# Performance work log

Hardware: AMD Instinct MI355X
Metric: run time of the kernel (lower is better)

The kernel has to match this reference:

```python
import jax, jax.numpy as jnp
import numpy as np

B, T = 16384, 2048
NUM_TOKENS = 60   # |A5| = 60
ID_ID = 0         # identity element id
LOGIT_VAL = 5.0


def setup_inputs() -> dict:
    key = jax.random.key(0)
    k1, k2 = jax.random.split(key)
    input_ids = jax.random.randint(k1, (B, T), 0, NUM_TOKENS, dtype=jnp.int32)
    # Cayley table: mul[a, b] = a*b in the group. Any table with entries in
    # [0, 60) exercises identical compute; a real A5 table would be passed here.
    mul = jax.random.randint(k2, (NUM_TOKENS, NUM_TOKENS), 0, NUM_TOKENS, dtype=jnp.int32)
    return {"input_ids": input_ids, "mul": mul}


def reference(input_ids, mul):
    # Sequential left-fold over timesteps: s_{t+1} = mul[x_t, s_t]
    Bv = input_ids.shape[0]

    def step(s, xt):
        return mul[xt, s], None  # per-row gather mul[xt[i], s[i]]

    s0 = jnp.full((Bv,), ID_ID, dtype=input_ids.dtype)
    s, _ = jax.lax.scan(step, s0, input_ids.T)  # scan over T; carries [B]

    # one-hot logits scaled to 5.0 (torch scatter_ of constant 5.0)
    logits = jnp.zeros((Bv, NUM_TOKENS), dtype=jnp.float32)
    logits = logits.at[jnp.arange(Bv), s].set(LOGIT_VAL)
    return logits
```

## Files before the change

kernel.cpp:

```cpp
#include <hip/hip_runtime.h>


#define T_LEN 2048
#define NTOK 60
#define NPAIR (NTOK * NTOK)
#define ROW_WORDS 675
#define NWORDS (NTOK * ROW_WORDS)
#define ALLOC_WORDS (NWORDS + 4)
#define TAB_BYTES (ALLOC_WORDS * 4)
#define BROWS 64

__global__ void a5_build_kernel(const int* __restrict__ mul,
                                uint32_t* __restrict__ packed) {
  const int w = blockIdx.x * 256 + threadIdx.x;
  if (w >= ALLOC_WORDS) return;
  if (w >= NWORDS) { packed[w] = 0; return; }
  const uint32_t r = (uint32_t)w / ROW_WORDS;
  const uint32_t woff = (uint32_t)w - r * ROW_WORDS;
  const uint32_t bit0 = woff * 32u;
  const uint32_t e0 = bit0 / 6u;
  const uint32_t sh0 = bit0 - e0 * 6u;
  uint64_t acc = 0;
#pragma unroll
  for (int k = 0; k < 7; ++k) {
    const uint32_t e = e0 + k;
    if (e < NPAIR) {
      const uint32_t x1 = e % 60u;
      const uint32_t x2 = e / 60u;
      const uint32_t v =
          (uint32_t)mul[x2 * 60u + (uint32_t)mul[x1 * 60u + r]];
      acc |= (uint64_t)v << (6 * k);
    }
  }
  packed[w] = (uint32_t)(acc >> sh0);
}

__global__ __launch_bounds__(BROWS)
__attribute__((amdgpu_waves_per_eu(1, 1)))
void a5_scan2_kernel(const int* __restrict__ ids,
                     const uint32_t* __restrict__ packed,
                     float* __restrict__ out) {
  extern __shared__ uint32_t tab[];
  const int lane = threadIdx.x;

  {
    const uint4* s4 = (const uint4*)packed;
    uint4* d4 = (uint4*)tab;
#pragma unroll 4
    for (int i = lane; i < ALLOC_WORDS / 4; i += BROWS) d4[i] = s4[i];
  }
  __syncthreads();

  const int row = blockIdx.x * BROWS + lane;
  const int4* rp = (const int4*)(ids + (size_t)row * T_LEN);
  const char* tb = (const char*)tab;

  uint32_t s = 0;
  uint32_t po[8], shv[8];

#define PREP(J, X1, X2)                                           \
  do {                                                            \
    const uint32_t p6_ = (uint32_t)(X2)*360u + (uint32_t)(X1)*6u; \
    po[J] = (p6_ >> 5) << 2;                                      \
    shv[J] = p6_ & 31u;                                           \
  } while (0)

#define PSTEP(J)                                                  \
  do {                                                            \
    const uint32_t a_ = s * 2700u + po[J];                        \
    const uint32_t lo_ = *(const uint32_t*)(tb + a_);             \
    const uint32_t hi_ = *(const uint32_t*)(tb + a_ + 4);         \
    s = __builtin_amdgcn_alignbit(hi_, lo_, shv[J]) & 63u;        \
  } while (0)

  int4 n0, n1, n2, n3;
  {
    int4 c0 = rp[0], c1 = rp[1], c2 = rp[2], c3 = rp[3];
    PREP(0, c0.x, c0.y); PREP(1, c0.z, c0.w);
    PREP(2, c1.x, c1.y); PREP(3, c1.z, c1.w);
    PREP(4, c2.x, c2.y); PREP(5, c2.z, c2.w);
    PREP(6, c3.x, c3.y); PREP(7, c3.z, c3.w);
    n0 = rp[4]; n1 = rp[5]; n2 = rp[6]; n3 = rp[7];
  }

  for (int b = 0; b <= 125; ++b) {
    const int4* mp = rp + (size_t)(b + 2) * 4;
    int4 m0 = mp[0], m1 = mp[1], m2 = mp[2], m3 = mp[3];
    __builtin_amdgcn_sched_barrier(0);
    PSTEP(0); PSTEP(1); PSTEP(2); PSTEP(3);
    PSTEP(4); PSTEP(5); PSTEP(6); PSTEP(7);
    __builtin_amdgcn_sched_barrier(0);
    PREP(0, n0.x, n0.y); PREP(1, n0.z, n0.w);
    PREP(2, n1.x, n1.y); PREP(3, n1.z, n1.w);
    PREP(4, n2.x, n2.y); PREP(5, n2.z, n2.w);
    PREP(6, n3.x, n3.y); PREP(7, n3.z, n3.w);
    n0 = m0; n1 = m1; n2 = m2; n3 = m3;
  }
  PSTEP(0); PSTEP(1); PSTEP(2); PSTEP(3);
  PSTEP(4); PSTEP(5); PSTEP(6); PSTEP(7);
  PREP(0, n0.x, n0.y); PREP(1, n0.z, n0.w);
  PREP(2, n1.x, n1.y); PREP(3, n1.z, n1.w);
  PREP(4, n2.x, n2.y); PREP(5, n2.z, n2.w);
  PREP(6, n3.x, n3.y); PREP(7, n3.z, n3.w);
  PSTEP(0); PSTEP(1); PSTEP(2); PSTEP(3);
  PSTEP(4); PSTEP(5); PSTEP(6); PSTEP(7);
#undef PSTEP
#undef PREP

  float4* op = (float4*)(out + (size_t)row * NTOK);
#pragma unroll
  for (int j = 0; j < 15; ++j) {
    float4 v;
    v.x = ((uint32_t)(4 * j + 0) == s) ? 5.0f : 0.0f;
    v.y = ((uint32_t)(4 * j + 1) == s) ? 5.0f : 0.0f;
    v.z = ((uint32_t)(4 * j + 2) == s) ? 5.0f : 0.0f;
    v.w = ((uint32_t)(4 * j + 3) == s) ? 5.0f : 0.0f;
    op[j] = v;
  }
}

__global__ __launch_bounds__(BROWS, 1) void a5_scan_kernel(
    const int* __restrict__ ids, const int* __restrict__ mul,
    float* __restrict__ out) {
  __shared__ uint32_t tab[NTOK * NTOK];
  const int lane = threadIdx.x;
  for (int i = lane; i < NTOK * NTOK; i += BROWS)
    tab[i] = ((uint32_t)mul[i]) << 2;
  __syncthreads();

  const int row = blockIdx.x * BROWS + lane;
  const int4* rp = (const int4*)(ids + (size_t)row * T_LEN);
  const char* tb = (const char*)tab;
  int4 c0 = rp[0], c1 = rp[1], c2 = rp[2], c3 = rp[3];
  uint32_t s4 = 0;
#define STEP(X)                                  \
  do {                                           \
    uint32_t base_ = (uint32_t)(X)*240u;         \
    s4 = *(const uint32_t*)(tb + base_ + s4);    \
  } while (0)
  for (int t = 0; t < T_LEN; t += 16) {
    int4 q0, q1, q2, q3;
    const bool more = (t + 16) < T_LEN;
    if (more) {
      const int4* np = rp + (t >> 2) + 4;
      q0 = np[0]; q1 = np[1]; q2 = np[2]; q3 = np[3];
    }
    STEP(c0.x); STEP(c0.y); STEP(c0.z); STEP(c0.w);
    STEP(c1.x); STEP(c1.y); STEP(c1.z); STEP(c1.w);
    STEP(c2.x); STEP(c2.y); STEP(c2.z); STEP(c2.w);
    STEP(c3.x); STEP(c3.y); STEP(c3.z); STEP(c3.w);
    if (more) { c0 = q0; c1 = q1; c2 = q2; c3 = q3; }
  }
#undef STEP
  const uint32_t s = s4 >> 2;
  float4* op = (float4*)(out + (size_t)row * NTOK);
#pragma unroll
  for (int j = 0; j < 15; ++j) {
    float4 v;
    v.x = ((uint32_t)(4 * j + 0) == s) ? 5.0f : 0.0f;
    v.y = ((uint32_t)(4 * j + 1) == s) ? 5.0f : 0.0f;
    v.z = ((uint32_t)(4 * j + 2) == s) ? 5.0f : 0.0f;
    v.w = ((uint32_t)(4 * j + 3) == s) ? 5.0f : 0.0f;
    op[j] = v;
  }
}

extern "C" void kernel_launch(void* const* d_in, const int* in_sizes, int n_in,
                              void* d_out, int out_size, void* d_ws,
                              size_t ws_size, hipStream_t stream) {
  const int* ids = (const int*)d_in[0];
  const int* mul = (const int*)d_in[1];
  float* out = (float*)d_out;
  const int B = in_sizes[0] / T_LEN;
  const int grid = B / BROWS;

  if (ws_size >= (size_t)TAB_BYTES) {
    uint32_t* packed = (uint32_t*)d_ws;
    (void)hipFuncSetAttribute((const void*)a5_scan2_kernel,
                              hipFuncAttributeMaxDynamicSharedMemorySize,
                              TAB_BYTES);
    a5_build_kernel<<<(ALLOC_WORDS + 255) / 256, 256, 0, stream>>>(mul, packed);
    a5_scan2_kernel<<<grid, BROWS, TAB_BYTES, stream>>>(ids, packed, out);
  } else {
    a5_scan_kernel<<<grid, BROWS, 0, stream>>>(ids, mul, out);
  }
}
```

Measured before the change: 84.81 us.

## Process two independent rows per thread to interleave dependent LDS lookup chains

Each thread now scans two rows (tid and tid+8192) and alternates their dependent shared-memory lookup steps, so two independent chains hide each other's LDS latency. The grid is halved, which also halves the number of times the ~162KB packed table is copied into LDS. The cost is roughly double the register pressure and only 128 blocks on a GPU with many more CUs, which may leave compute units idle. The fast path now also requires B to equal exactly 16384.

```diff
diff --git a/kernel.cpp b/kernel.cpp
--- a/kernel.cpp
+++ b/kernel.cpp
@@ -9,6 +9,7 @@
 #define ALLOC_WORDS (NWORDS + 4)
 #define TAB_BYTES (ALLOC_WORDS * 4)
 #define BROWS 64
+#define HALF_B 8192
 
 __global__ void a5_build_kernel(const int* __restrict__ mul,
                                 uint32_t* __restrict__ packed) {
@@ -37,9 +38,9 @@
 
 __global__ __launch_bounds__(BROWS)
 __attribute__((amdgpu_waves_per_eu(1, 1)))
-void a5_scan2_kernel(const int* __restrict__ ids,
-                     const uint32_t* __restrict__ packed,
-                     float* __restrict__ out) {
+void a5_scan2x2_kernel(const int* __restrict__ ids,
+                       const uint32_t* __restrict__ packed,
+                       float* __restrict__ out) {
   extern __shared__ uint32_t tab[];
   const int lane = threadIdx.x;
 
@@ -51,71 +52,114 @@
   }
   __syncthreads();
 
-  const int row = blockIdx.x * BROWS + lane;
-  const int4* rp = (const int4*)(ids + (size_t)row * T_LEN);
+  const int tid = blockIdx.x * BROWS + lane;
+  const int4* rpA = (const int4*)(ids + (size_t)tid * T_LEN);
+  const int4* rpB = (const int4*)(ids + (size_t)(tid + HALF_B) * T_LEN);
   const char* tb = (const char*)tab;
 
-  uint32_t s = 0;
-  uint32_t po[8], shv[8];
-
-#define PREP(J, X1, X2)                                           \
+  uint32_t sA = 0, sB = 0;
+  uint32_t poA[8], shA[8], poB[8], shB[8];
+
+#define PREPC(PO, SH, J, X1, X2)                                  \
   do {                                                            \
     const uint32_t p6_ = (uint32_t)(X2)*360u + (uint32_t)(X1)*6u; \
-    po[J] = (p6_ >> 5) << 2;                                      \
-    shv[J] = p6_ & 31u;                                           \
+    PO[J] = (p6_ >> 5) << 2;                                      \
+    SH[J] = p6_ & 31u;                                            \
   } while (0)
 
-#define PSTEP(J)                                                  \
+#define PSTEPC(S, PO, SH, J)                                      \
   do {                                                            \
-    const uint32_t a_ = s * 2700u + po[J];                        \
+    const uint32_t a_ = S * 2700u + PO[J];                        \
     const uint32_t lo_ = *(const uint32_t*)(tb + a_);             \
     const uint32_t hi_ = *(const uint32_t*)(tb + a_ + 4);         \
-    s = __builtin_amdgcn_alignbit(hi_, lo_, shv[J]) & 63u;        \
+    S = __builtin_amdgcn_alignbit(hi_, lo_, SH[J]) & 63u;         \
   } while (0)
 
-  int4 n0, n1, n2, n3;
+  int4 nA0, nA1, nA2, nA3, nB0, nB1, nB2, nB3;
   {
-    int4 c0 = rp[0], c1 = rp[1], c2 = rp[2], c3 = rp[3];
-    PREP(0, c0.x, c0.y); PREP(1, c0.z, c0.w);
-    PREP(2, c1.x, c1.y); PREP(3, c1.z, c1.w);
-    PREP(4, c2.x, c2.y); PREP(5, c2.z, c2.w);
-    PREP(6, c3.x, c3.y); PREP(7, c3.z, c3.w);
-    n0 = rp[4]; n1 = rp[5]; n2 = rp[6]; n3 = rp[7];
+    int4 c0 = rpA[0], c1 = rpA[1], c2 = rpA[2], c3 = rpA[3];
+    PREPC(poA, shA, 0, c0.x, c0.y); PREPC(poA, shA, 1, c0.z, c0.w);
+    PREPC(poA, shA, 2, c1.x, c1.y); PREPC(poA, shA, 3, c1.z, c1.w);
+    PREPC(poA, shA, 4, c2.x, c2.y); PREPC(poA, shA, 5, c2.z, c2.w);
+    PREPC(poA, shA, 6, c3.x, c3.y); PREPC(poA, shA, 7, c3.z, c3.w);
+    int4 d0 = rpB[0], d1 = rpB[1], d2 = rpB[2], d3 = rpB[3];
+    PREPC(poB, shB, 0, d0.x, d0.y); PREPC(poB, shB, 1, d0.z, d0.w);
+    PREPC(poB, shB, 2, d1.x, d1.y); PREPC(poB, shB, 3, d1.z, d1.w);
+    PREPC(poB, shB, 4, d2.x, d2.y); PREPC(poB, shB, 5, d2.z, d2.w);
+    PREPC(poB, shB, 6, d3.x, d3.y); PREPC(poB, shB, 7, d3.z, d3.w);
+    nA0 = rpA[4]; nA1 = rpA[5]; nA2 = rpA[6]; nA3 = rpA[7];
+    nB0 = rpB[4]; nB1 = rpB[5]; nB2 = rpB[6]; nB3 = rpB[7];
   }
 
   for (int b = 0; b <= 125; ++b) {
-    const int4* mp = rp + (size_t)(b + 2) * 4;
-    int4 m0 = mp[0], m1 = mp[1], m2 = mp[2], m3 = mp[3];
+    const int4* mpA = rpA + (size_t)(b + 2) * 4;
+    const int4* mpB = rpB + (size_t)(b + 2) * 4;
+    int4 mA0 = mpA[0], mA1 = mpA[1], mA2 = mpA[2], mA3 = mpA[3];
+    int4 mB0 = mpB[0], mB1 = mpB[1], mB2 = mpB[2], mB3 = mpB[3];
     __builtin_amdgcn_sched_barrier(0);
-    PSTEP(0); PSTEP(1); PSTEP(2); PSTEP(3);
-    PSTEP(4); PSTEP(5); PSTEP(6); PSTEP(7);
+    PSTEPC(sA, poA, shA, 0); PSTEPC(sB, poB, shB, 0);
+    PSTEPC(sA, poA, shA, 1); PSTEPC(sB, poB, shB, 1);
+    PSTEPC(sA, poA, shA, 2); PSTEPC(sB, poB, shB, 2);
+    PSTEPC(sA, poA, shA, 3); PSTEPC(sB, poB, shB, 3);
+    PSTEPC(sA, poA, shA, 4); PSTEPC(sB, poB, shB, 4);
+    PSTEPC(sA, poA, shA, 5); PSTEPC(sB, poB, shB, 5);
+    PSTEPC(sA, poA, shA, 6); PSTEPC(sB, poB, shB, 6);
+    PSTEPC(sA, poA, shA, 7); PSTEPC(sB, poB, shB, 7);
     __builtin_amdgcn_sched_barrier(0);
-    PREP(0, n0.x, n0.y); PREP(1, n0.z, n0.w);
-    PREP(2, n1.x, n1.y); PREP(3, n1.z, n1.w);
-    PREP(4, n2.x, n2.y); PREP(5, n2.z, n2.w);
-    PREP(6, n3.x, n3.y); PREP(7, n3.z, n3.w);
-    n0 = m0; n1 = m1; n2 = m2; n3 = m3;
-  }
-  PSTEP(0); PSTEP(1); PSTEP(2); PSTEP(3);
-  PSTEP(4); PSTEP(5); PSTEP(6); PSTEP(7);
-  PREP(0, n0.x, n0.y); PREP(1, n0.z, n0.w);
-  PREP(2, n1.x, n1.y); PREP(3, n1.z, n1.w);
-  PREP(4, n2.x, n2.y); PREP(5, n2.z, n2.w);
-  PREP(6, n3.x, n3.y); PREP(7, n3.z, n3.w);
-  PSTEP(0); PSTEP(1); PSTEP(2); PSTEP(3);
-  PSTEP(4); PSTEP(5); PSTEP(6); PSTEP(7);
-#undef PSTEP
-#undef PREP
-
-  float4* op = (float4*)(out + (size_t)row * NTOK);
+    PREPC(poA, shA, 0, nA0.x, nA0.y); PREPC(poA, shA, 1, nA0.z, nA0.w);
+    PREPC(poA, shA, 2, nA1.x, nA1.y); PREPC(poA, shA, 3, nA1.z, nA1.w);
+    PREPC(poA, shA, 4, nA2.x, nA2.y); PREPC(poA, shA, 5, nA2.z, nA2.w);
+    PREPC(poA, shA, 6, nA3.x, nA3.y); PREPC(poA, shA, 7, nA3.z, nA3.w);
+    PREPC(poB, shB, 0, nB0.x, nB0.y); PREPC(poB, shB, 1, nB0.z, nB0.w);
+    PREPC(poB, shB, 2, nB1.x, nB1.y); PREPC(poB, shB, 3, nB1.z, nB1.w);
+    PREPC(poB, shB, 4, nB2.x, nB2.y); PREPC(poB, shB, 5, nB2.z, nB2.w);
+    PREPC(poB, shB, 6, nB3.x, nB3.y); PREPC(poB, shB, 7, nB3.z, nB3.w);
+    nA0 = mA0; nA1 = mA1; nA2 = mA2; nA3 = mA3;
+    nB0 = mB0; nB1 = mB1; nB2 = mB2; nB3 = mB3;
+  }
+  PSTEPC(sA, poA, shA, 0); PSTEPC(sB, poB, shB, 0);
+  PSTEPC(sA, poA, shA, 1); PSTEPC(sB, poB, shB, 1);
+  PSTEPC(sA, poA, shA, 2); PSTEPC(sB, poB, shB, 2);
+  PSTEPC(sA, poA, shA, 3); PSTEPC(sB, poB, shB, 3);
+  PSTEPC(sA, poA, shA, 4); PSTEPC(sB, poB, shB, 4);
+  PSTEPC(sA, poA, shA, 5); PSTEPC(sB, poB, shB, 5);
+  PSTEPC(sA, poA, shA, 6); PSTEPC(sB, poB, shB, 6);
+  PSTEPC(sA, poA, shA, 7); PSTEPC(sB, poB, shB, 7);
+  PREPC(poA, shA, 0, nA0.x, nA0.y); PREPC(poA, shA, 1, nA0.z, nA0.w);
+  PREPC(poA, shA, 2, nA1.x, nA1.y); PREPC(poA, shA, 3, nA1.z, nA1.w);
+  PREPC(poA, shA, 4, nA2.x, nA2.y); PREPC(poA, shA, 5, nA2.z, nA2.w);
+  PREPC(poA, shA, 6, nA3.x, nA3.y); PREPC(poA, shA, 7, nA3.z, nA3.w);
+  PREPC(poB, shB, 0, nB0.x, nB0.y); PREPC(poB, shB, 1, nB0.z, nB0.w);
+  PREPC(poB, shB, 2, nB1.x, nB1.y); PREPC(poB, shB, 3, nB1.z, nB1.w);
+  PREPC(poB, shB, 4, nB2.x, nB2.y); PREPC(poB, shB, 5, nB2.z, nB2.w);
+  PREPC(poB, shB, 6, nB3.x, nB3.y); PREPC(poB, shB, 7, nB3.z, nB3.w);
+  PSTEPC(sA, poA, shA, 0); PSTEPC(sB, poB, shB, 0);
+  PSTEPC(sA, poA, shA, 1); PSTEPC(sB, poB, shB, 1);
+  PSTEPC(sA, poA, shA, 2); PSTEPC(sB, poB, shB, 2);
+  PSTEPC(sA, poA, shA, 3); PSTEPC(sB, poB, shB, 3);
+  PSTEPC(sA, poA, shA, 4); PSTEPC(sB, poB, shB, 4);
+  PSTEPC(sA, poA, shA, 5); PSTEPC(sB, poB, shB, 5);
+  PSTEPC(sA, poA, shA, 6); PSTEPC(sB, poB, shB, 6);
+  PSTEPC(sA, poA, shA, 7); PSTEPC(sB, poB, shB, 7);
+#undef PSTEPC
+#undef PREPC
+
+  float4* opA = (float4*)(out + (size_t)tid * NTOK);
+  float4* opB = (float4*)(out + (size_t)(tid + HALF_B) * NTOK);
 #pragma unroll
   for (int j = 0; j < 15; ++j) {
     float4 v;
-    v.x = ((uint32_t)(4 * j + 0) == s) ? 5.0f : 0.0f;
-    v.y = ((uint32_t)(4 * j + 1) == s) ? 5.0f : 0.0f;
-    v.z = ((uint32_t)(4 * j + 2) == s) ? 5.0f : 0.0f;
-    v.w = ((uint32_t)(4 * j + 3) == s) ? 5.0f : 0.0f;
-    op[j] = v;
+    v.x = ((uint32_t)(4 * j + 0) == sA) ? 5.0f : 0.0f;
+    v.y = ((uint32_t)(4 * j + 1) == sA) ? 5.0f : 0.0f;
+    v.z = ((uint32_t)(4 * j + 2) == sA) ? 5.0f : 0.0f;
+    v.w = ((uint32_t)(4 * j + 3) == sA) ? 5.0f : 0.0f;
+    opA[j] = v;
+    float4 w;
+    w.x = ((uint32_t)(4 * j + 0) == sB) ? 5.0f : 0.0f;
+    w.y = ((uint32_t)(4 * j + 1) == sB) ? 5.0f : 0.0f;
+    w.z = ((uint32_t)(4 * j + 2) == sB) ? 5.0f : 0.0f;
+    w.w = ((uint32_t)(4 * j + 3) == sB) ? 5.0f : 0.0f;
+    opB[j] = w;
   }
 }
 
@@ -172,16 +216,16 @@
   const int* mul = (const int*)d_in[1];
   float* out = (float*)d_out;
   const int B = in_sizes[0] / T_LEN;
-  const int grid = B / BROWS;
-
-  if (ws_size >= (size_t)TAB_BYTES) {
+
+  if (ws_size >= (size_t)TAB_BYTES && B == 2 * HALF_B) {
     uint32_t* packed = (uint32_t*)d_ws;
-    (void)hipFuncSetAttribute((const void*)a5_scan2_kernel,
+    (void)hipFuncSetAttribute((const void*)a5_scan2x2_kernel,
                               hipFuncAttributeMaxDynamicSharedMemorySize,
                               TAB_BYTES);
     a5_build_kernel<<<(ALLOC_WORDS + 255) / 256, 256, 0, stream>>>(mul, packed);
-    a5_scan2_kernel<<<grid, BROWS, TAB_BYTES, stream>>>(ids, packed, out);
+    a5_scan2x2_kernel<<<HALF_B / BROWS, BROWS, TAB_BYTES, stream>>>(ids, packed,
+                                                                    out);
   } else {
-    a5_scan_kernel<<<grid, BROWS, 0, stream>>>(ids, mul, out);
-  }
-}
+    a5_scan_kernel<<<B / BROWS, BROWS, 0, stream>>>(ids, mul, out);
+  }
+}
```

Result: slower. 103.0 us (+21.5%).
